# Performance work log

Measured on AMD Instinct MI355X. Metric: run time of the kernel, lower is better.

## Reference

```python
import jax, jax.numpy as jnp
import numpy as np

DIM = 1024
H = 16
HD = DIM // H  # 64
B = 2
S = 2048


def setup_inputs() -> dict:
    key = jax.random.key(0)
    ks = jax.random.split(key, 8)
    return {
        "x": jax.random.normal(ks[0], (B, S, DIM), dtype=jnp.float32),
        "memory": jax.random.normal(ks[1], (B, H, HD, HD), dtype=jnp.float32),
        "norm": jax.random.uniform(ks[2], (B, H, HD), dtype=jnp.float32),
        "Wq": jax.random.normal(ks[3], (DIM, DIM), dtype=jnp.float32) * (DIM ** -0.5),
        "Wk": jax.random.normal(ks[4], (DIM, DIM), dtype=jnp.float32) * (DIM ** -0.5),
        "Wv": jax.random.normal(ks[5], (DIM, DIM), dtype=jnp.float32) * (DIM ** -0.5),
        "Wo": jax.random.normal(ks[6], (DIM, DIM), dtype=jnp.float32) * (DIM ** -0.5),
        "gate": jnp.zeros((1, H, 1, 1), dtype=jnp.float32),
    }


def reference(x, memory, norm, Wq, Wk, Wv, Wo, gate):
    b, s, _ = x.shape
    scale = HD ** -0.5
    # projections (torch Linear: y = x @ W.T), split heads -> [b,h,s,hd]
    def proj(W):
        return jnp.einsum('bsd,ed->bse', x, W).reshape(b, s, H, HD).transpose(0, 2, 1, 3)
    q = proj(Wq)
    k = proj(Wk)
    v = proj(Wv)
    # causal local attention
    scores = jnp.einsum('bhqd,bhkd->bhqk', q, k) * scale
    causal = jnp.tril(jnp.ones((s, s), dtype=bool))  # True = keep
    scores = jnp.where(causal, scores, jnp.finfo(scores.dtype).min)
    attn = jax.nn.softmax(scores, axis=-1)
    local_out = jnp.einsum('bhqk,bhkd->bhqd', attn, v)
    # compressive memory read
    q_mem = jax.nn.elu(q) + 1.0  # positive features
    mem_out = jnp.einsum('bhsd,bhde->bhse', q_mem, memory)
    normalizer = jnp.einsum('bhsd,bhd->bhs', q_mem, norm)[..., None] + 1e-6
    mem_out = mem_out / normalizer
    # gated combine
    g = jax.nn.sigmoid(gate)
    combined = g * mem_out + (1.0 - g) * local_out
    # memory write
    k_mem = jax.nn.elu(k) + 1.0
    new_memory = memory + jnp.einsum('bhsd,bhse->bhde', k_mem, v)
    new_norm = norm + k_mem.sum(axis=2)
    # merge heads + output projection
    out = combined.transpose(0, 2, 1, 3).reshape(b, s, DIM)
    out = jnp.einsum('bsd,ed->bse', out, Wo)
    return out, new_memory, new_norm
```

## Files before the change

### kernel.cpp

```cpp
#include <hip/hip_runtime.h>
#include <hip/hip_bf16.h>
#include <math.h>
#include <type_traits>

#define DIM 1024
#define NH 16
#define HD 64
#define NB 2
#define SEQ 2048

typedef unsigned short u16;
typedef short short8 __attribute__((ext_vector_type(8)));
typedef unsigned short u16x8 __attribute__((ext_vector_type(8)));
typedef unsigned short u16x4v __attribute__((ext_vector_type(4)));
typedef float f32x4 __attribute__((ext_vector_type(4)));

#define LOG2E 1.44269504f

__device__ __forceinline__ u16 f2bf(float f) {
    __hip_bfloat16 h = __float2bfloat16(f);
    return __builtin_bit_cast(u16, h);
}
__device__ __forceinline__ float bf2f(u16 u) {
    return __uint_as_float(((unsigned)u) << 16);
}
__device__ __forceinline__ u16 f2bf_trunc(float f) {
    return (u16)(__float_as_uint(f) >> 16);
}
__device__ __forceinline__ float fast_exp2(float x) {
    float r;
    asm("v_exp_f32 %0, %1" : "=v"(r) : "v"(x));
    return r;
}

__device__ __forceinline__ void gload_lds16(const u16* g, u16* l) {
    __builtin_amdgcn_global_load_lds(
        (const __attribute__((address_space(1))) unsigned int*)g,
        (__attribute__((address_space(3))) unsigned int*)l, 16, 0, 0);
}

__global__ __launch_bounds__(256)
void conv_bf16(const float* __restrict__ x,
               const float* __restrict__ wq, const float* __restrict__ wk,
               const float* __restrict__ wv, const float* __restrict__ wo,
               u16* __restrict__ xbf, u16* __restrict__ wbf)
{
    const int idx8 = (blockIdx.x * 256 + threadIdx.x) * 8;
    const float* src; u16* dst; int off;
    if (idx8 < (1 << 22)) {
        src = x; dst = xbf; off = idx8;
    } else {
        const int wi  = idx8 - (1 << 22);
        const int sel = wi >> 20;
        src = (sel == 0) ? wq : (sel == 1) ? wk : (sel == 2) ? wv : wo;
        dst = wbf + ((size_t)sel << 20);
        off = wi & ((1 << 20) - 1);
    }
    float4 a = *(const float4*)(src + off);
    float4 b = *(const float4*)(src + off + 4);
    u16x8 o;
    o[0] = f2bf(a.x); o[1] = f2bf(a.y); o[2] = f2bf(a.z); o[3] = f2bf(a.w);
    o[4] = f2bf(b.x); o[5] = f2bf(b.y); o[6] = f2bf(b.z); o[7] = f2bf(b.w);
    *(u16x8*)(dst + off) = o;
}

template<int MODE, int FM>
__global__ __launch_bounds__(256)
void gemm_lds(const u16* __restrict__ X, const u16* __restrict__ Wall,
              u16* __restrict__ Obf, float* __restrict__ Of,
              const float* __restrict__ part, const float* __restrict__ pnorm,
              const float* __restrict__ memv, const float* __restrict__ normv,
              float* __restrict__ new_mem, float* __restrict__ new_norm)
{
    constexpr int MT = FM * 32;
    __shared__ u16 As[MT * 64];
    __shared__ u16 Bs[128 * 64];

    if (MODE == 1 && blockIdx.y == 8) {
        if (blockIdx.x >= 32) return;
        const int bh = blockIdx.x;
        const int t  = threadIdx.x;
        #pragma unroll
        for (int u = 0; u < 16; ++u) {
            const int fl = t + (u << 8);
            float s = memv[(size_t)bh * 4096 + fl];
            #pragma unroll
            for (int ch = 0; ch < 16; ++ch)
                s += part[((size_t)bh * 16 + ch) * 4096 + fl];
            new_mem[(size_t)bh * 4096 + fl] = s;
        }
        if (t < 64) {
            float s = normv[(size_t)bh * 64 + t];
            #pragma unroll
            for (int ch = 0; ch < 16; ++ch)
                s += pnorm[((size_t)bh * 16 + ch) * 64 + t];
            new_norm[(size_t)bh * 64 + t] = s;
        }
        return;
    }

    const int t    = threadIdx.x;
    const int lane = t & 63;
    const int wave = t >> 6;
    const int wm = wave >> 1, wn = wave & 1;
    const int lr = lane & 15, kg = lane >> 4;
    const int m_base = blockIdx.x * MT;
    const int n_base = blockIdx.y * 128;

    const u16* Xb = X + (size_t)m_base * DIM;
    const u16* Wb = Wall + (MODE == 0 ? ((size_t)blockIdx.z << 20) : (size_t)0)
                         + (size_t)n_base * DIM;

    f32x4 acc[FM][4];
    #pragma unroll
    for (int i = 0; i < FM; ++i)
        #pragma unroll
        for (int j = 0; j < 4; ++j) {
            f32x4 z = {0.f, 0.f, 0.f, 0.f};
            acc[i][j] = z;
        }

    for (int k0 = 0; k0 < DIM; k0 += 64) {
        __syncthreads();
        #pragma unroll
        for (int u = 0; u < FM; ++u) {
            const int cid = (u << 8) + t;
            const int row = cid >> 3, c16 = cid & 7;
            const int src = c16 ^ (row & 7);
            gload_lds16(Xb + (size_t)row * DIM + k0 + (src << 3), &As[cid << 3]);
        }
        #pragma unroll
        for (int u = 0; u < 4; ++u) {
            const int cid = (u << 8) + t;
            const int row = cid >> 3, c16 = cid & 7;
            const int src = c16 ^ (row & 7);
            gload_lds16(Wb + (size_t)row * DIM + k0 + (src << 3), &Bs[cid << 3]);
        }
        __syncthreads();

        #pragma unroll
        for (int kh = 0; kh < 2; ++kh) {
            short8 afrag[FM], bfrag[4];
            #pragma unroll
            for (int fm = 0; fm < FM; ++fm) {
                const int r = wm * (FM * 16) + fm * 16 + lr;
                const int c = (kh << 2) + kg;
                afrag[fm] = *(const short8*)&As[r * 64 + (((c) ^ (r & 7)) << 3)];
            }
            #pragma unroll
            for (int fn = 0; fn < 4; ++fn) {
                const int r = wn * 64 + fn * 16 + lr;
                const int c = (kh << 2) + kg;
                bfrag[fn] = *(const short8*)&Bs[r * 64 + (((c) ^ (r & 7)) << 3)];
            }
            #pragma unroll
            for (int fm = 0; fm < FM; ++fm)
                #pragma unroll
                for (int fn = 0; fn < 4; ++fn)
                    acc[fm][fn] = __builtin_amdgcn_mfma_f32_16x16x32_bf16(
                        afrag[fm], bfrag[fn], acc[fm][fn], 0, 0, 0);
        }
    }

    u16* O0 = (MODE == 0) ? Obf + ((size_t)blockIdx.z << 22) : nullptr;
    if (MODE == 0 && blockIdx.z == 2) {
        #pragma unroll
        for (int fm = 0; fm < FM; ++fm) {
            const int m0 = m_base + wm * (FM * 16) + fm * 16 + kg * 4;
            const int b_ = m0 >> 11;
            const int s0 = m0 & (SEQ - 1);
            #pragma unroll
            for (int fn = 0; fn < 4; ++fn) {
                const int n  = n_base + wn * 64 + fn * 16 + lr;
                const int h_ = n >> 6, d_ = n & 63;
                u16x4v pk;
                #pragma unroll
                for (int i = 0; i < 4; ++i) pk[i] = f2bf(acc[fm][fn][i]);
                *(u16x4v*)(O0 + (((size_t)b_ * NH + h_) * HD + d_) * SEQ + s0) = pk;
            }
        }
    } else {
        #pragma unroll
        for (int fm = 0; fm < FM; ++fm) {
            const int mrow0 = m_base + wm * (FM * 16) + fm * 16 + kg * 4;
            #pragma unroll
            for (int i = 0; i < 4; ++i) {
                const int m = mrow0 + i;
                const int b = m >> 11;
                const int s = m & (SEQ - 1);
                #pragma unroll
                for (int fn = 0; fn < 4; ++fn) {
                    const int n = n_base + wn * 64 + fn * 16 + lr;
                    const float val = acc[fm][fn][i];
                    if (MODE == 0)
                        O0[(((size_t)b * NH + (n >> 6)) * SEQ + s) * HD + (n & 63)] =
                            f2bf(val);
                    else
                        Of[((size_t)b * SEQ + s) * DIM + n] = val;
                }
            }
        }
    }
}

__global__ __launch_bounds__(256, 2)
void attn_mfma(const u16* __restrict__ q,
               const u16* __restrict__ k,
               const u16* __restrict__ vt,
               const float* __restrict__ memv,
               const float* __restrict__ normv,
               const float* __restrict__ gatev,
               u16* __restrict__ comb)
{
    __shared__ u16 Ks[3][64 * 64];
    __shared__ u16 Vs[3][64 * 64];
    __shared__ u16 Ps[4 * 16 * 64];

    const int t    = threadIdx.x;
    const int lane = t & 63;
    const int w    = t >> 6;
    const int lr   = lane & 15;
    const int kg   = lane >> 4;

    const int lin  = blockIdx.x + 16 * blockIdx.y + 256 * blockIdx.z;
    const int x    = lin & 7;
    const int gg   = lin >> 3;
    const int bh_i = x + 8 * (gg & 3);
    const int p    = gg >> 2;
    const int h    = bh_i & 15;
    const int b    = bh_i >> 4;
    const int qa = p, qb = 31 - p;
    const int nkt = qb + 1;

    const size_t bh = (size_t)b * NH + h;
    const u16* qp  = q  + bh * SEQ * HD;
    const u16* kp  = k  + bh * SEQ * HD;
    const u16* vtp = vt + bh * SEQ * HD;

    int koff[4][2];
    #pragma unroll
    for (int fn = 0; fn < 4; ++fn)
        #pragma unroll
        for (int kk = 0; kk < 2; ++kk) {
            const int r = fn * 16 + lr;
            koff[fn][kk] = r * 64 + ((((kk << 2) + kg) ^ (r & 7)) << 3);
        }
    int pwoff[4][4];
    #pragma unroll
    for (int r = 0; r < 4; ++r) {
        const int row_p = kg * 4 + r;
        const int base_r = w * 1024 + row_p * 64 + (lr & 7);
        #pragma unroll
        for (int fn = 0; fn < 4; ++fn)
            pwoff[r][fn] = base_r + ((((fn << 1) + (lr >> 3)) ^ (row_p & 7)) << 3);
    }
    int pfoff[2];
    #pragma unroll
    for (int kk = 0; kk < 2; ++kk)
        pfoff[kk] = w * 1024 + lr * 64 + ((((kk << 2) + kg) ^ (lr & 7)) << 3);

    auto stageK = [&](int kt, u16* dst) {
        #pragma unroll
        for (int u = 0; u < 2; ++u) {
            const int cid = (u << 8) + t;
            const int row = cid >> 3, c16 = cid & 7;
            const int src = c16 ^ (row & 7);
            gload_lds16(kp + (size_t)(kt * 64 + row) * HD + (src << 3),
                        dst + (cid << 3));
        }
    };
    auto stageV = [&](int kt, u16* dst) {
        #pragma unroll
        for (int u = 0; u < 2; ++u) {
            const int cid = (u << 8) + t;
            const int row = cid >> 3, c16 = cid & 7;
            const int src = c16 ^ (row & 7);
            gload_lds16(vtp + (size_t)row * SEQ + kt * 64 + (src << 3),
                        dst + (cid << 3));
        }
    };

    float* norm_s = (float*)Ps;
    if (t < 64) norm_s[t] = normv[bh * HD + t];
    __syncthreads();

    const int rb2[2] = {qa * 64 + w * 16, qb * 64 + w * 16};
    short8 qatt[2][2], qmem[2][2];
    float nrrow[2];
    #pragma unroll
    for (int fm = 0; fm < 2; ++fm) {
        const u16* qrow = qp + (size_t)(rb2[fm] + lr) * HD;
        float nr = 0.f;
        #pragma unroll
        for (int kk = 0; kk < 2; ++kk) {
            const int dbase = kk * 32 + kg * 8;
            u16x8 raw = *(const u16x8*)(qrow + dbase);
            short8 sa, sm;
            #pragma unroll
            for (int i = 0; i < 8; ++i) {
                const float xx = bf2f(raw[i]);
                sa[i] = (short)f2bf(xx * (0.125f * LOG2E));
                const float e = (xx > 0.f) ? (xx + 1.f) : __expf(xx);
                sm[i] = (short)f2bf(e);
                nr = fmaf(e, norm_s[dbase + i], nr);
            }
            qatt[fm][kk] = sa; qmem[fm][kk] = sm;
        }
        nr += __shfl_xor(nr, 16);
        nr += __shfl_xor(nr, 32);
        nrrow[fm] = nr;
    }

    short8 ones8;
    {
        const short o = (lr == 0) ? (short)0x3F80 : (short)0;
        #pragma unroll
        for (int i = 0; i < 8; ++i) ones8[i] = o;
    }

    f32x4 oacc[2][4], lacc[2];
    #pragma unroll
    for (int fm = 0; fm < 2; ++fm) {
        #pragma unroll
        for (int fn = 0; fn < 4; ++fn) {
            f32x4 z = {0.f, 0.f, 0.f, 0.f};
            oacc[fm][fn] = z;
        }
        f32x4 z = {0.f, 0.f, 0.f, 0.f};
        lacc[fm] = z;
    }

    stageK(0, &Ks[0][0]);
    stageV(0, &Vs[0][0]);
    if (nkt > 1) {
        stageK(1, &Ks[1][0]);
        stageV(1, &Vs[1][0]);
        asm volatile("s_waitcnt vmcnt(4)" ::: "memory");
    } else {
        asm volatile("s_waitcnt vmcnt(0)" ::: "memory");
    }
    __builtin_amdgcn_sched_barrier(0);
    __builtin_amdgcn_s_barrier();

    int cur = 0;
    for (int kt = 0; kt < nkt; ++kt) {
        const u16* Kc = &Ks[cur][0];
        const u16* Vc = &Vs[cur][0];
        const int sl2 = (cur == 0) ? 2 : cur - 1;

        const bool more2 = (kt + 2 < nkt);
        if (more2) {
            stageK(kt + 2, &Ks[sl2][0]);
            stageV(kt + 2, &Vs[sl2][0]);
        }

        short8 kf[4][2], vf[4][2];
        #pragma unroll
        for (int fn = 0; fn < 4; ++fn)
            #pragma unroll
            for (int kk = 0; kk < 2; ++kk) {
                kf[fn][kk] = *(const short8*)&Kc[koff[fn][kk]];
                vf[fn][kk] = *(const short8*)&Vc[koff[fn][kk]];
            }

        auto do_fm = [&](auto FMC) {
            constexpr int fm = FMC.value;
            const int rb = rb2[fm];
            const bool diag = (kt == (fm ? qb : qa));
            f32x4 S[4];
            #pragma unroll
            for (int fn = 0; fn < 4; ++fn) {
                f32x4 z = {0.f, 0.f, 0.f, 0.f};
                S[fn] = z;
            }
            __builtin_amdgcn_s_setprio(1);
            #pragma unroll
            for (int fn = 0; fn < 4; ++fn)
                #pragma unroll
                for (int kk = 0; kk < 2; ++kk)
                    S[fn] = __builtin_amdgcn_mfma_f32_16x16x32_bf16(
                        qatt[fm][kk], kf[fn][kk], S[fn], 0, 0, 0);
            __builtin_amdgcn_s_setprio(0);

            #pragma unroll
            for (int fn = 0; fn < 4; ++fn) {
                const int kgl = kt * 64 + fn * 16 + lr;
                #pragma unroll
                for (int r = 0; r < 4; ++r) {
                    float pe = fast_exp2(S[fn][r]);
                    if (diag && kgl > rb + kg * 4 + r) pe = 0.f;
                    Ps[pwoff[r][fn]] = f2bf_trunc(pe);
                }
            }

            short8 pf[2];
            #pragma unroll
            for (int kk = 0; kk < 2; ++kk)
                pf[kk] = *(const short8*)&Ps[pfoff[kk]];
            __builtin_amdgcn_s_setprio(1);
            #pragma unroll
            for (int fnd = 0; fnd < 4; ++fnd)
                #pragma unroll
                for (int kk = 0; kk < 2; ++kk)
                    oacc[fm][fnd] = __builtin_amdgcn_mfma_f32_16x16x32_bf16(
                        pf[kk], vf[fnd][kk], oacc[fm][fnd], 0, 0, 0);
            #pragma unroll
            for (int kk = 0; kk < 2; ++kk)
                lacc[fm] = __builtin_amdgcn_mfma_f32_16x16x32_bf16(
                    pf[kk], ones8, lacc[fm], 0, 0, 0);
            __builtin_amdgcn_s_setprio(0);
        };
        if (kt <= qa) do_fm(std::integral_constant<int, 0>{});
        do_fm(std::integral_constant<int, 1>{});

        if (more2) {
            asm volatile("s_waitcnt vmcnt(4)" ::: "memory");
        } else {
            asm volatile("s_waitcnt vmcnt(0)" ::: "memory");
        }
        __builtin_amdgcn_sched_barrier(0);
        __builtin_amdgcn_s_barrier();

        cur = (cur == 2) ? 0 : cur + 1;
    }

    u16* MtS = Ps;
    {
        const float* Mb = memv + bh * HD * HD;
        #pragma unroll
        for (int u = 0; u < 2; ++u) {
            const int cid = (u << 8) + t;
            const int gd = cid & 63;
            const int e0 = (cid >> 6) << 3;
            float4 m0 = *(const float4*)(Mb + gd * HD + e0);
            float4 m1 = *(const float4*)(Mb + gd * HD + e0 + 4);
            float mv8[8];
            *(float4*)&mv8[0] = m0; *(float4*)&mv8[4] = m1;
            const int a = gd >> 3, bse = gd & 7;
            #pragma unroll
            for (int j = 0; j < 8; ++j)
                MtS[(e0 + j) * 64 + ((a ^ j) << 3) + bse] = f2bf(mv8[j]);
        }
    }
    __syncthreads();

    short8 mf2[4][2];
    #pragma unroll
    for (int fn = 0; fn < 4; ++fn)
        #pragma unroll
        for (int kk = 0; kk < 2; ++kk)
            mf2[fn][kk] = *(const short8*)&MtS[koff[fn][kk]];

    const float gte = gatev[h];
    const float g  = 1.f / (1.f + __expf(-gte));
    const float og = 1.f - g;

    #pragma unroll
    for (int fm = 0; fm < 2; ++fm) {
        f32x4 macc[4];
        #pragma unroll
        for (int fn = 0; fn < 4; ++fn) {
            f32x4 z = {0.f, 0.f, 0.f, 0.f};
            macc[fn] = z;
            #pragma unroll
            for (int kk = 0; kk < 2; ++kk)
                macc[fn] = __builtin_amdgcn_mfma_f32_16x16x32_bf16(
                    qmem[fm][kk], mf2[fn][kk], macc[fn], 0, 0, 0);
        }
        #pragma unroll
        for (int r = 0; r < 4; ++r) {
            const int rt  = kg * 4 + r;
            const float lsum  = __shfl(lacc[fm][r], lane & 48);
            const float linv  = 1.f / lsum;
            const float nrd   = __shfl(nrrow[fm], (lane & 48) | rt);
            const float nrinv = 1.f / (nrd + 1e-6f);
            const int qg = rb2[fm] + rt;
            u16* crow = comb + ((size_t)b * SEQ + qg) * DIM + h * HD;
            #pragma unroll
            for (int fn = 0; fn < 4; ++fn)
                crow[fn * 16 + lr] = f2bf(
                    g * (macc[fn][r] * nrinv) + og * (oacc[fm][fn][r] * linv));
        }
    }
}

__global__ __launch_bounds__(256)
void memwrite_mfma(const u16* __restrict__ k,
                   const u16* __restrict__ vt,
                   float* __restrict__ part,
                   float* __restrict__ pnorm)
{
    __shared__ u16 KelT[64 * 64];
    __shared__ u16 Vs[64 * 64];

    const int ch = blockIdx.x;
    const int bh = blockIdx.y;
    const int t    = threadIdx.x;
    const int lane = t & 63;
    const int w    = t >> 6;
    const int lr   = lane & 15;
    const int kg   = lane >> 4;

    const u16* kb  = k  + (size_t)bh * SEQ * HD + (size_t)ch * 128 * HD;
    const u16* vtb = vt + (size_t)bh * SEQ * HD + (size_t)ch * 128;

    int aoff[2];
    #pragma unroll
    for (int kk = 0; kk < 2; ++kk) {
        const int r = w * 16 + lr;
        aoff[kk] = r * 64 + ((((kk << 2) + kg) ^ (r & 7)) << 3);
    }
    int boff[4][2];
    #pragma unroll
    for (int fn = 0; fn < 4; ++fn)
        #pragma unroll
        for (int kk = 0; kk < 2; ++kk) {
            const int r = fn * 16 + lr;
            boff[fn][kk] = r * 64 + ((((kk << 2) + kg) ^ (r & 7)) << 3);
        }

    short8 ones8;
    {
        const short o = (lr == 0) ? (short)0x3F80 : (short)0;
        #pragma unroll
        for (int i = 0; i < 8; ++i) ones8[i] = o;
    }

    f32x4 acc[4], lacc;
    #pragma unroll
    for (int fn = 0; fn < 4; ++fn) {
        f32x4 z = {0.f, 0.f, 0.f, 0.f};
        acc[fn] = z;
    }
    { f32x4 z = {0.f, 0.f, 0.f, 0.f}; lacc = z; }

    for (int st = 0; st < 2; ++st) {
        __syncthreads();
        #pragma unroll
        for (int u = 0; u < 2; ++u) {
            const int cid = (u << 8) + t;
            const int row = cid >> 3, c16 = cid & 7;
            const int src = c16 ^ (row & 7);
            gload_lds16(vtb + (size_t)row * SEQ + st * 64 + (src << 3),
                        &Vs[cid << 3]);
        }
        #pragma unroll
        for (int u = 0; u < 2; ++u) {
            const int cid = (u << 8) + t;
            const int krow = cid & 63;
            const int d0   = (cid >> 6) << 3;
            u16x8 kv = *(const u16x8*)(kb + (size_t)(st * 64 + krow) * HD + d0);
            const int a = krow >> 3, bse = krow & 7;
            #pragma unroll
            for (int j = 0; j < 8; ++j) {
                const float kf = bf2f(kv[j]);
                const float e = (kf > 0.f) ? kf + 1.f : __expf(kf);
                KelT[(d0 + j) * 64 + ((a ^ ((d0 + j) & 7)) << 3) + bse] = f2bf(e);
            }
        }
        __syncthreads();

        short8 af[2];
        #pragma unroll
        for (int kk = 0; kk < 2; ++kk)
            af[kk] = *(const short8*)&KelT[aoff[kk]];
        #pragma unroll
        for (int fn = 0; fn < 4; ++fn)
            #pragma unroll
            for (int kk = 0; kk < 2; ++kk) {
                short8 bfv = *(const short8*)&Vs[boff[fn][kk]];
                acc[fn] = __builtin_amdgcn_mfma_f32_16x16x32_bf16(
                    af[kk], bfv, acc[fn], 0, 0, 0);
            }
        #pragma unroll
        for (int kk = 0; kk < 2; ++kk)
            lacc = __builtin_amdgcn_mfma_f32_16x16x32_bf16(
                af[kk], ones8, lacc, 0, 0, 0);
    }

    float* po = part + ((size_t)bh * 16 + ch) * 4096;
    #pragma unroll
    for (int r = 0; r < 4; ++r) {
        const int d = w * 16 + kg * 4 + r;
        #pragma unroll
        for (int fn = 0; fn < 4; ++fn)
            po[d * 64 + fn * 16 + lr] = acc[fn][r];
    }
    if (lr == 0) {
        #pragma unroll
        for (int r = 0; r < 4; ++r)
            pnorm[((size_t)bh * 16 + ch) * 64 + w * 16 + kg * 4 + r] = lacc[r];
    }
}

extern "C" void kernel_launch(void* const* d_in, const int* in_sizes, int n_in,
                              void* d_out, int out_size, void* d_ws, size_t ws_size,
                              hipStream_t stream)
{
    const float* x     = (const float*)d_in[0];
    const float* memv  = (const float*)d_in[1];
    const float* normv = (const float*)d_in[2];
    const float* Wq    = (const float*)d_in[3];
    const float* Wk    = (const float*)d_in[4];
    const float* Wv    = (const float*)d_in[5];
    const float* Wo    = (const float*)d_in[6];
    const float* gate  = (const float*)d_in[7];
    float* out = (float*)d_out;

    u16* xbf  = (u16*)d_ws;
    u16* wbf  = xbf + ((size_t)1 << 22);
    u16* qkv  = wbf + ((size_t)4 << 20);
    u16* comb = qkv + ((size_t)3 << 22);
    float* part  = (float*)(comb + ((size_t)1 << 22));
    float* pnorm = part + ((size_t)1 << 21);

    u16* qbf = qkv;
    u16* kbf = qkv + ((size_t)1 << 22);
    u16* vtb = qkv + ((size_t)2 << 22);

    float* new_mem  = out + (size_t)NB * SEQ * DIM;
    float* new_norm = new_mem + (size_t)NB * NH * HD * HD;

    conv_bf16<<<dim3(4096), 256, 0, stream>>>(x, Wq, Wk, Wv, Wo, xbf, wbf);
    gemm_lds<0, 4><<<dim3(32, 8, 3), 256, 0, stream>>>(
        xbf, wbf, qkv, nullptr,
        nullptr, nullptr, nullptr, nullptr, nullptr, nullptr);
    attn_mfma<<<dim3(16, 16, 2), 256, 0, stream>>>(qbf, kbf, vtb, memv, normv,
                                                   gate, comb);
    memwrite_mfma<<<dim3(16, 32), 256, 0, stream>>>(kbf, vtb, part, pnorm);
    gemm_lds<1, 2><<<dim3(64, 9, 1), 256, 0, stream>>>(
        comb, wbf + ((size_t)3 << 20), nullptr, out,
        part, pnorm, memv, normv, new_mem, new_norm);
}
```

Before: 116.6 us.

## Split attention query tiles across 8 waves instead of 4 per block

The attention kernel moves from 256 to 512 threads per block. Each wave now owns a single 16-row slice of one of the two paired query tiles, where before each wave processed both tiles. Staging loops, register arrays and the epilogue are simplified to match, cutting per-wave registers and doubling waves in flight. The trade-off is that waves owning the short (qa) tile sit idle for later key tiles while still joining every barrier, and the larger block may reduce how many blocks fit per CU.

```diff
diff --git a/kernel.cpp b/kernel.cpp
--- a/kernel.cpp
+++ b/kernel.cpp
@@ -203,7 +203,7 @@
     }
 }
 
-__global__ __launch_bounds__(256, 2)
+__global__ __launch_bounds__(512, 2)
 void attn_mfma(const u16* __restrict__ q,
                const u16* __restrict__ k,
                const u16* __restrict__ vt,
@@ -214,7 +214,7 @@
 {
     __shared__ u16 Ks[3][64 * 64];
     __shared__ u16 Vs[3][64 * 64];
-    __shared__ u16 Ps[4 * 16 * 64];
+    __shared__ u16 Ps[8 * 16 * 64];
 
     const int t    = threadIdx.x;
     const int lane = t & 63;
@@ -232,6 +232,11 @@
     const int qa = p, qb = 31 - p;
     const int nkt = qb + 1;
 
+    const int fm  = w >> 2;
+    const int w4  = w & 3;
+    const int myq = fm ? qb : qa;
+    const int rb  = myq * 64 + w4 * 16;
+
     const size_t bh = (size_t)b * NH + h;
     const u16* qp  = q  + bh * SEQ * HD;
     const u16* kp  = k  + bh * SEQ * HD;
@@ -260,36 +265,26 @@
         pfoff[kk] = w * 1024 + lr * 64 + ((((kk << 2) + kg) ^ (lr & 7)) << 3);
 
     auto stageK = [&](int kt, u16* dst) {
-        #pragma unroll
-        for (int u = 0; u < 2; ++u) {
-            const int cid = (u << 8) + t;
-            const int row = cid >> 3, c16 = cid & 7;
-            const int src = c16 ^ (row & 7);
-            gload_lds16(kp + (size_t)(kt * 64 + row) * HD + (src << 3),
-                        dst + (cid << 3));
-        }
+        const int row = t >> 3, c16 = t & 7;
+        const int src = c16 ^ (row & 7);
+        gload_lds16(kp + (size_t)(kt * 64 + row) * HD + (src << 3),
+                    dst + (t << 3));
     };
     auto stageV = [&](int kt, u16* dst) {
-        #pragma unroll
-        for (int u = 0; u < 2; ++u) {
-            const int cid = (u << 8) + t;
-            const int row = cid >> 3, c16 = cid & 7;
-            const int src = c16 ^ (row & 7);
-            gload_lds16(vtp + (size_t)row * SEQ + kt * 64 + (src << 3),
-                        dst + (cid << 3));
-        }
+        const int row = t >> 3, c16 = t & 7;
+        const int src = c16 ^ (row & 7);
+        gload_lds16(vtp + (size_t)row * SEQ + kt * 64 + (src << 3),
+                    dst + (t << 3));
     };
 
     float* norm_s = (float*)Ps;
     if (t < 64) norm_s[t] = normv[bh * HD + t];
     __syncthreads();
 
-    const int rb2[2] = {qa * 64 + w * 16, qb * 64 + w * 16};
-    short8 qatt[2][2], qmem[2][2];
-    float nrrow[2];
-    #pragma unroll
-    for (int fm = 0; fm < 2; ++fm) {
-        const u16* qrow = qp + (size_t)(rb2[fm] + lr) * HD;
+    short8 qatt[2], qmem[2];
+    float nrrow;
+    {
+        const u16* qrow = qp + (size_t)(rb + lr) * HD;
         float nr = 0.f;
         #pragma unroll
         for (int kk = 0; kk < 2; ++kk) {
@@ -304,11 +299,11 @@
                 sm[i] = (short)f2bf(e);
                 nr = fmaf(e, norm_s[dbase + i], nr);
             }
-            qatt[fm][kk] = sa; qmem[fm][kk] = sm;
+            qatt[kk] = sa; qmem[kk] = sm;
         }
         nr += __shfl_xor(nr, 16);
         nr += __shfl_xor(nr, 32);
-        nrrow[fm] = nr;
+        nrrow = nr;
     }
 
     short8 ones8;
@@ -318,27 +313,19 @@
         for (int i = 0; i < 8; ++i) ones8[i] = o;
     }
 
-    f32x4 oacc[2][4], lacc[2];
-    #pragma unroll
-    for (int fm = 0; fm < 2; ++fm) {
-        #pragma unroll
-        for (int fn = 0; fn < 4; ++fn) {
-            f32x4 z = {0.f, 0.f, 0.f, 0.f};
-            oacc[fm][fn] = z;
-        }
+    f32x4 oacc[4], lacc;
+    #pragma unroll
+    for (int fn = 0; fn < 4; ++fn) {
         f32x4 z = {0.f, 0.f, 0.f, 0.f};
-        lacc[fm] = z;
-    }
+        oacc[fn] = z;
+    }
+    { f32x4 z = {0.f, 0.f, 0.f, 0.f}; lacc = z; }
 
     stageK(0, &Ks[0][0]);
     stageV(0, &Vs[0][0]);
-    if (nkt > 1) {
-        stageK(1, &Ks[1][0]);
-        stageV(1, &Vs[1][0]);
-        asm volatile("s_waitcnt vmcnt(4)" ::: "memory");
-    } else {
-        asm volatile("s_waitcnt vmcnt(0)" ::: "memory");
-    }
+    stageK(1, &Ks[1][0]);
+    stageV(1, &Vs[1][0]);
+    asm volatile("s_waitcnt vmcnt(2)" ::: "memory");
     __builtin_amdgcn_sched_barrier(0);
     __builtin_amdgcn_s_barrier();
 
@@ -354,19 +341,17 @@
             stageV(kt + 2, &Vs[sl2][0]);
         }
 
-        short8 kf[4][2], vf[4][2];
-        #pragma unroll
-        for (int fn = 0; fn < 4; ++fn)
-            #pragma unroll
-            for (int kk = 0; kk < 2; ++kk) {
-                kf[fn][kk] = *(const short8*)&Kc[koff[fn][kk]];
-                vf[fn][kk] = *(const short8*)&Vc[koff[fn][kk]];
-            }
-
-        auto do_fm = [&](auto FMC) {
-            constexpr int fm = FMC.value;
-            const int rb = rb2[fm];
-            const bool diag = (kt == (fm ? qb : qa));
+        if (kt <= myq) {
+            short8 kf[4][2], vf[4][2];
+            #pragma unroll
+            for (int fn = 0; fn < 4; ++fn)
+                #pragma unroll
+                for (int kk = 0; kk < 2; ++kk) {
+                    kf[fn][kk] = *(const short8*)&Kc[koff[fn][kk]];
+                    vf[fn][kk] = *(const short8*)&Vc[koff[fn][kk]];
+                }
+
+            const bool diag = (kt == myq);
             f32x4 S[4];
             #pragma unroll
             for (int fn = 0; fn < 4; ++fn) {
@@ -379,7 +364,7 @@
                 #pragma unroll
                 for (int kk = 0; kk < 2; ++kk)
                     S[fn] = __builtin_amdgcn_mfma_f32_16x16x32_bf16(
-                        qatt[fm][kk], kf[fn][kk], S[fn], 0, 0, 0);
+                        qatt[kk], kf[fn][kk], S[fn], 0, 0, 0);
             __builtin_amdgcn_s_setprio(0);
 
             #pragma unroll
@@ -402,19 +387,17 @@
             for (int fnd = 0; fnd < 4; ++fnd)
                 #pragma unroll
                 for (int kk = 0; kk < 2; ++kk)
-                    oacc[fm][fnd] = __builtin_amdgcn_mfma_f32_16x16x32_bf16(
-                        pf[kk], vf[fnd][kk], oacc[fm][fnd], 0, 0, 0);
+                    oacc[fnd] = __builtin_amdgcn_mfma_f32_16x16x32_bf16(
+                        pf[kk], vf[fnd][kk], oacc[fnd], 0, 0, 0);
             #pragma unroll
             for (int kk = 0; kk < 2; ++kk)
-                lacc[fm] = __builtin_amdgcn_mfma_f32_16x16x32_bf16(
-                    pf[kk], ones8, lacc[fm], 0, 0, 0);
+                lacc = __builtin_amdgcn_mfma_f32_16x16x32_bf16(
+                    pf[kk], ones8, lacc, 0, 0, 0);
             __builtin_amdgcn_s_setprio(0);
-        };
-        if (kt <= qa) do_fm(std::integral_constant<int, 0>{});
-        do_fm(std::integral_constant<int, 1>{});
+        }
 
         if (more2) {
-            asm volatile("s_waitcnt vmcnt(4)" ::: "memory");
+            asm volatile("s_waitcnt vmcnt(2)" ::: "memory");
         } else {
             asm volatile("s_waitcnt vmcnt(0)" ::: "memory");
         }
@@ -427,20 +410,16 @@
     u16* MtS = Ps;
     {
         const float* Mb = memv + bh * HD * HD;
-        #pragma unroll
-        for (int u = 0; u < 2; ++u) {
-            const int cid = (u << 8) + t;
-            const int gd = cid & 63;
-            const int e0 = (cid >> 6) << 3;
-            float4 m0 = *(const float4*)(Mb + gd * HD + e0);
-            float4 m1 = *(const float4*)(Mb + gd * HD + e0 + 4);
-            float mv8[8];
-            *(float4*)&mv8[0] = m0; *(float4*)&mv8[4] = m1;
-            const int a = gd >> 3, bse = gd & 7;
-            #pragma unroll
-            for (int j = 0; j < 8; ++j)
-                MtS[(e0 + j) * 64 + ((a ^ j) << 3) + bse] = f2bf(mv8[j]);
-        }
+        const int gd = t & 63;
+        const int e0 = (t >> 6) << 3;
+        float4 m0 = *(const float4*)(Mb + gd * HD + e0);
+        float4 m1 = *(const float4*)(Mb + gd * HD + e0 + 4);
+        float mv8[8];
+        *(float4*)&mv8[0] = m0; *(float4*)&mv8[4] = m1;
+        const int a = gd >> 3, bse = gd & 7;
+        #pragma unroll
+        for (int j = 0; j < 8; ++j)
+            MtS[(e0 + j) * 64 + ((a ^ j) << 3) + bse] = f2bf(mv8[j]);
     }
     __syncthreads();
 
@@ -455,32 +434,30 @@
     const float g  = 1.f / (1.f + __expf(-gte));
     const float og = 1.f - g;
 
-    #pragma unroll
-    for (int fm = 0; fm < 2; ++fm) {
-        f32x4 macc[4];
-        #pragma unroll
-        for (int fn = 0; fn < 4; ++fn) {
-            f32x4 z = {0.f, 0.f, 0.f, 0.f};
-            macc[fn] = z;
-            #pragma unroll
-            for (int kk = 0; kk < 2; ++kk)
-                macc[fn] = __builtin_amdgcn_mfma_f32_16x16x32_bf16(
-                    qmem[fm][kk], mf2[fn][kk], macc[fn], 0, 0, 0);
-        }
-        #pragma unroll
-        for (int r = 0; r < 4; ++r) {
-            const int rt  = kg * 4 + r;
-            const float lsum  = __shfl(lacc[fm][r], lane & 48);
-            const float linv  = 1.f / lsum;
-            const float nrd   = __shfl(nrrow[fm], (lane & 48) | rt);
-            const float nrinv = 1.f / (nrd + 1e-6f);
-            const int qg = rb2[fm] + rt;
-            u16* crow = comb + ((size_t)b * SEQ + qg) * DIM + h * HD;
-            #pragma unroll
-            for (int fn = 0; fn < 4; ++fn)
-                crow[fn * 16 + lr] = f2bf(
-                    g * (macc[fn][r] * nrinv) + og * (oacc[fm][fn][r] * linv));
-        }
+    f32x4 macc[4];
+    #pragma unroll
+    for (int fn = 0; fn < 4; ++fn) {
+        f32x4 z = {0.f, 0.f, 0.f, 0.f};
+        macc[fn] = z;
+        #pragma unroll
+        for (int kk = 0; kk < 2; ++kk)
+            macc[fn] = __builtin_amdgcn_mfma_f32_16x16x32_bf16(
+                qmem[kk], mf2[fn][kk], macc[fn], 0, 0, 0);
+    }
+
+    #pragma unroll
+    for (int r = 0; r < 4; ++r) {
+        const int rt  = kg * 4 + r;
+        const float lsum  = __shfl(lacc[r], lane & 48);
+        const float linv  = 1.f / lsum;
+        const float nrd   = __shfl(nrrow, (lane & 48) | rt);
+        const float nrinv = 1.f / (nrd + 1e-6f);
+        const int qg = rb + rt;
+        u16* crow = comb + ((size_t)b * SEQ + qg) * DIM + h * HD;
+        #pragma unroll
+        for (int fn = 0; fn < 4; ++fn)
+            crow[fn * 16 + lr] = f2bf(
+                g * (macc[fn][r] * nrinv) + og * (oacc[fn][r] * linv));
     }
 }
 
@@ -625,7 +602,7 @@
     gemm_lds<0, 4><<<dim3(32, 8, 3), 256, 0, stream>>>(
         xbf, wbf, qkv, nullptr,
         nullptr, nullptr, nullptr, nullptr, nullptr, nullptr);
-    attn_mfma<<<dim3(16, 16, 2), 256, 0, stream>>>(qbf, kbf, vtb, memv, normv,
+    attn_mfma<<<dim3(16, 16, 2), 512, 0, stream>>>(qbf, kbf, vtb, memv, normv,
                                                    gate, comb);
     memwrite_mfma<<<dim3(16, 32), 256, 0, stream>>>(kbf, vtb, part, pnorm);
     gemm_lds<1, 2><<<dim3(64, 9, 1), 256, 0, stream>>>(
```

New measurement: 140.1 us. 20.2% more time.
